# Kernel optimization log

Measured on AMD Instinct MI355X. Metric: run time of the kernel, lower is better.

Reference implementation:

```python
import jax, jax.numpy as jnp
import numpy as np

NUM_HEADS = 32
HEAD_DIM = 32  # hard-coded in the module


def _rope_sincos(seq_len, head_dim):
    # NOTE: module uses arange(0, head_dim)/head_dim (full dim, not the usual /2 stride)
    inv_freq = 1.0 / (10000.0 ** (jnp.arange(0, head_dim, dtype=jnp.float32) / head_dim))
    freqs = jnp.outer(jnp.arange(seq_len, dtype=jnp.float32), inv_freq)  # [S, D]
    # original repeats over heads then reshapes -> identical values per head,
    # so broadcasting with shape [1, S, 1, D] is equivalent.
    return jnp.sin(freqs)[None, :, None, :], jnp.cos(freqs)[None, :, None, :]


def _apply_rope(x, sin, cos):
    x1, x2 = jnp.split(x, 2, axis=-1)
    x_rot = jnp.concatenate([-x2, x1], axis=-1)
    return x * cos + x_rot * sin


def setup_inputs() -> dict:
    key = jax.random.key(0)
    B, S, H, D = 2, 2048, NUM_HEADS, HEAD_DIM
    dm = H * D
    k1, k2 = jax.random.split(key)
    x = jax.random.normal(k1, (B, S, dm), dtype=jnp.float32)
    W_qkv = jax.random.normal(k2, (dm, 3 * dm), dtype=jnp.float32) / np.sqrt(dm).astype(np.float32)
    mask = jnp.tril(jnp.ones((S, S), dtype=bool))[None, None]  # causal, [1,1,S,S]
    return {"x": x, "W_qkv": W_qkv, "mask": mask}


def reference(x, W_qkv, mask):
    B, S, dm = x.shape
    H, D = NUM_HEADS, HEAD_DIM
    qkv = x @ W_qkv  # [B, S, 3*H*D], no bias
    q, k, v = jnp.split(qkv, 3, axis=-1)
    q = q.reshape(B, S, H, D)
    k = k.reshape(B, S, H, D)
    v = v.reshape(B, S, H, D)

    sin, cos = _rope_sincos(S, D)
    q = _apply_rope(q, sin, cos)
    k = _apply_rope(k, sin, cos)

    # [B, H, S, D]
    q = q.transpose(0, 2, 1, 3)
    k = k.transpose(0, 2, 1, 3)
    v = v.transpose(0, 2, 1, 3)

    scale = 1.0 / np.sqrt(D).astype(np.float32)
    attn = jnp.einsum('bhqd,bhkd->bhqk', q, k) * scale  # [B, H, S, S]
    attn = jnp.where(mask, attn, jnp.float32(-jnp.inf))
    attn = jax.nn.softmax(attn, axis=-1)
    out = jnp.einsum('bhqk,bhkd->bhqd', attn, v)  # [B, H, S, D]
    return out.transpose(0, 2, 1, 3).reshape(B, S, H * D)
```

## Files before the change

### kernel.cpp

```cpp
#include <hip/hip_runtime.h>
#include <cstdint>
#include <cstddef>

#define BB 2
#define SS 2048
#define HH 32
#define DD 32
#define DM 1024
#define MROWS 4096
#define NQKV 3072

#define QSCALE 0.25503486f

typedef __attribute__((ext_vector_type(8))) short bf16x8;
typedef __attribute__((ext_vector_type(4))) float f32x4;
typedef __attribute__((address_space(1))) unsigned int gu32;
typedef __attribute__((address_space(3))) unsigned int lu32;

__device__ __forceinline__ unsigned short f2bf(float f) {
    union { float f; unsigned int u; } v;
    v.f = f;
    unsigned int u = v.u;
    u += 0x7fffu + ((u >> 16) & 1u);
    return (unsigned short)(u >> 16);
}

__device__ __forceinline__ unsigned int cvt_pk_bf16(float a, float b) {
    unsigned int r;
    asm("v_cvt_pk_bf16_f32 %0, %1, %2" : "=v"(r) : "v"(a), "v"(b));
    return r;
}
__device__ __forceinline__ unsigned short bf1(float a) {
    return (unsigned short)cvt_pk_bf16(a, a);
}

__global__ __launch_bounds__(256) void prep_k(
        const float* __restrict__ x, const float* __restrict__ w,
        unsigned short* __restrict__ xb, unsigned short* __restrict__ wT,
        float* __restrict__ tk, float* __restrict__ tq) {
    __shared__ unsigned short tile[64][65];
    const int blk = blockIdx.x;
    const int tid = threadIdx.x;
    if (blk < 4096) {
        const int i = blk * 256 + tid;
        float4 v = ((const float4*)x)[i];
        ushort4 o;
        o.x = f2bf(v.x); o.y = f2bf(v.y); o.z = f2bf(v.z); o.w = f2bf(v.w);
        ((ushort4*)xb)[i] = o;
    } else if (blk < 4864) {
        const int bx = blk - 4096;
        const int n0 = (bx % 48) * 64;
        const int k0 = (bx / 48) * 64;
        const int tx = tid & 63;
        const int ty = tid >> 6;
        for (int i = ty; i < 64; i += 4)
            tile[i][tx] = f2bf(w[(size_t)(k0 + i) * NQKV + n0 + tx]);
        __syncthreads();
        for (int i = ty; i < 64; i += 4)
            wT[(size_t)(n0 + i) * 1024 + k0 + tx] = tile[tx][i];
    } else {
        const int i = (blk - 4864) * 256 + tid;
        const int s = i >> 4, dl = i & 15;
        const float inv1 = exp2f((float)dl * -0.41524101186092029f);
        const float inv2 = exp2f((float)(dl + 16) * -0.41524101186092029f);
        float s1, c1, s2, c2;
        sincosf((float)s * inv1, &s1, &c1);
        sincosf((float)s * inv2, &s2, &c2);
        float4 vk = {s1, c1, s2, c2};
        float4 vq = {s1 * QSCALE, c1 * QSCALE, s2 * QSCALE, c2 * QSCALE};
        ((float4*)tk)[i] = vk;
        ((float4*)tq)[i] = vq;
    }
}

__global__ __launch_bounds__(256) void qkv_gemm_k(
        const unsigned short* __restrict__ xb,
        const unsigned short* __restrict__ wTp,
        const float4* __restrict__ tk, const float4* __restrict__ tq,
        unsigned short* __restrict__ qbuf,
        unsigned short* __restrict__ kbuf,
        unsigned short* __restrict__ vtbuf) {
    __shared__ unsigned short smem[2 * 128 * 32];
    unsigned short* As = smem;
    unsigned short* Bs = smem + 4096;
    const int m0 = blockIdx.x * 128;
    const int n0 = blockIdx.y * 128;
    const int tid = threadIdx.x;
    const int w = tid >> 6, lane = tid & 63;
    const int quad = lane >> 4, l16 = lane & 15;
    const int wr = w >> 1, wc = w & 1;

    f32x4 acc[4][4];
#pragma unroll
    for (int i = 0; i < 4; ++i)
#pragma unroll
        for (int j = 0; j < 4; ++j)
            acc[i][j] = (f32x4){0.f, 0.f, 0.f, 0.f};

    const int goff = (lane >> 2) * 1024 + (((lane ^ (lane >> 3)) & 3)) * 8;
    const int Gr = l16 * 4 + quad;
    const int L = Gr ^ ((Gr >> 3) & 3);
    const int roff = L * 8;

    for (int k0 = 0; k0 < 1024; k0 += 32) {
        __syncthreads();
#pragma unroll
        for (int q = 0; q < 2; ++q) {
            const int seg = w * 2 + q;
            const unsigned short* ga = xb  + (size_t)(m0 + seg * 16) * 1024 + k0 + goff;
            const unsigned short* gb = wTp + (size_t)(n0 + seg * 16) * 1024 + k0 + goff;
            __builtin_amdgcn_global_load_lds((gu32*)ga, (lu32*)(As + seg * 512), 16, 0, 0);
            __builtin_amdgcn_global_load_lds((gu32*)gb, (lu32*)(Bs + seg * 512), 16, 0, 0);
        }
        __syncthreads();
        bf16x8 af[4], bfv[4];
#pragma unroll
        for (int i = 0; i < 4; ++i)
            af[i] = *(const bf16x8*)(As + (wr * 4 + i) * 512 + roff);
#pragma unroll
        for (int j = 0; j < 4; ++j)
            bfv[j] = *(const bf16x8*)(Bs + (wc * 4 + j) * 512 + roff);
#pragma unroll
        for (int i = 0; i < 4; ++i)
#pragma unroll
            for (int j = 0; j < 4; ++j)
                acc[i][j] = __builtin_amdgcn_mfma_f32_16x16x32_bf16(af[i], bfv[j], acc[i][j], 0, 0, 0);
    }

    const int sec = n0 >> 10;
    const int rowb = m0 + wr * 64;
    const int colb = n0 + wc * 64;
    if (sec < 2) {
        unsigned short* dst = (sec == 0) ? qbuf : kbuf;
        const float4* tab = (sec == 0) ? tq : tk;
        const int h0 = (colb & 1023) >> 5;
        const int h1 = ((colb + 32) & 1023) >> 5;
#pragma unroll
        for (int i = 0; i < 4; ++i) {
#pragma unroll
            for (int r = 0; r < 4; ++r) {
                const int row = rowb + i * 16 + quad * 4 + r;
                const int bb = row >> 11, s = row & 2047;
                const float4 t = tab[s * 16 + l16];
                unsigned short* pb = dst + ((size_t)(bb * 32) * 2048 + s) * 32;
                {
                    const float x1 = acc[i][0][r], x2 = acc[i][1][r];
                    unsigned short* p = pb + (size_t)h0 * (2048 * 32);
                    p[l16]      = bf1(x1 * t.y - x2 * t.x);
                    p[l16 + 16] = bf1(x2 * t.w + x1 * t.z);
                }
                {
                    const float x1 = acc[i][2][r], x2 = acc[i][3][r];
                    unsigned short* p = pb + (size_t)h1 * (2048 * 32);
                    p[l16]      = bf1(x1 * t.y - x2 * t.x);
                    p[l16 + 16] = bf1(x2 * t.w + x1 * t.z);
                }
            }
        }
    } else {
        __syncthreads();
        unsigned short* tw = smem + w * 2048;
        const int bbi = rowb >> 11;
        const int srow = rowb & 2047;
        const int colB = colb - 2048;
#pragma unroll
        for (int j = 0; j < 4; ++j) {
#pragma unroll
            for (int i = 0; i < 4; ++i) {
                uint2 pk;
                pk.x = cvt_pk_bf16(acc[i][j][0], acc[i][j][1]);
                pk.y = cvt_pk_bf16(acc[i][j][2], acc[i][j][3]);
                *(uint2*)&tw[l16 * 66 + i * 16 + quad * 4] = pk;
            }
#pragma unroll
            for (int c = 0; c < 16; ++c) {
                const int col = colB + j * 16 + c;
                const int hh = col >> 5, d = col & 31;
                vtbuf[((size_t)(bbi * 32 + hh) * 32 + d) * 2048 + srow + lane] = tw[c * 66 + lane];
            }
        }
    }
}

__global__ __launch_bounds__(256) void attn_k(
        const unsigned short* __restrict__ qb,
        const unsigned short* __restrict__ kb,
        const unsigned short* __restrict__ vt,
        float* __restrict__ out) {
    __shared__ unsigned short Pl[4][2][32][40];
    const int tid = threadIdx.x;
    const int w = tid >> 6, lane = tid & 63;
    const int quad = lane >> 4, l16 = lane & 15;
    const int bh = blockIdx.x >> 4;
    const int j = blockIdx.x & 15;
    const int b = bh >> 5, h = bh & 31;

    const int c = (w < 2) ? (2 * j + w) : (62 - 2 * j + (w - 2));
    const int qw = c * 32;
    const int nkt = c + 1;

    const unsigned short* qbase = qb + (size_t)bh * 2048 * 32;
    const unsigned short* kbase = kb + (size_t)bh * 2048 * 32;
    const unsigned short* vbase = vt + (size_t)bh * 32 * 2048;
    const f32x4 fz = {0.f, 0.f, 0.f, 0.f};

    bf16x8 qf0 = *(const bf16x8*)(qbase + (size_t)(qw + l16) * 32 + quad * 8);
    bf16x8 qf1 = *(const bf16x8*)(qbase + (size_t)(qw + 16 + l16) * 32 + quad * 8);

    f32x4 a00 = fz, a01 = fz, a10 = fz, a11 = fz;
    float ls0 = 0.f, ls1 = 0.f;

    const unsigned short* kp0 = kbase + (size_t)l16 * 32 + quad * 8;
    const unsigned short* kp1 = kbase + (size_t)(16 + l16) * 32 + quad * 8;
    const unsigned short* vp0 = vbase + (size_t)l16 * 2048 + quad * 8;
    const unsigned short* vp1 = vbase + (size_t)(16 + l16) * 2048 + quad * 8;

    bf16x8 kc0 = *(const bf16x8*)kp0;
    bf16x8 kc1 = *(const bf16x8*)kp1;
    bf16x8 vc0 = *(const bf16x8*)vp0;
    bf16x8 vc1 = *(const bf16x8*)vp1;

    for (int kt = 0; kt < nkt - 1; ++kt) {
        kp0 += 1024; kp1 += 1024; vp0 += 32; vp1 += 32;
        bf16x8 kn0 = *(const bf16x8*)kp0;
        bf16x8 kn1 = *(const bf16x8*)kp1;
        bf16x8 vn0 = *(const bf16x8*)vp0;
        bf16x8 vn1 = *(const bf16x8*)vp1;

        f32x4 s00 = __builtin_amdgcn_mfma_f32_16x16x32_bf16(kc0, qf0, fz, 0, 0, 0);
        f32x4 s01 = __builtin_amdgcn_mfma_f32_16x16x32_bf16(kc0, qf1, fz, 0, 0, 0);
        f32x4 s10 = __builtin_amdgcn_mfma_f32_16x16x32_bf16(kc1, qf0, fz, 0, 0, 0);
        f32x4 s11 = __builtin_amdgcn_mfma_f32_16x16x32_bf16(kc1, qf1, fz, 0, 0, 0);

        unsigned short (*plw)[40] = Pl[w][kt & 1];
        {
            float p0 = __builtin_amdgcn_exp2f(s00[0]), p1 = __builtin_amdgcn_exp2f(s00[1]);
            float p2 = __builtin_amdgcn_exp2f(s00[2]), p3 = __builtin_amdgcn_exp2f(s00[3]);
            ls0 += (p0 + p1) + (p2 + p3);
            uint2 pk; pk.x = cvt_pk_bf16(p0, p1); pk.y = cvt_pk_bf16(p2, p3);
            *(uint2*)&plw[l16][quad * 4] = pk;
        }
        {
            float p0 = __builtin_amdgcn_exp2f(s01[0]), p1 = __builtin_amdgcn_exp2f(s01[1]);
            float p2 = __builtin_amdgcn_exp2f(s01[2]), p3 = __builtin_amdgcn_exp2f(s01[3]);
            ls1 += (p0 + p1) + (p2 + p3);
            uint2 pk; pk.x = cvt_pk_bf16(p0, p1); pk.y = cvt_pk_bf16(p2, p3);
            *(uint2*)&plw[16 + l16][quad * 4] = pk;
        }
        {
            float p0 = __builtin_amdgcn_exp2f(s10[0]), p1 = __builtin_amdgcn_exp2f(s10[1]);
            float p2 = __builtin_amdgcn_exp2f(s10[2]), p3 = __builtin_amdgcn_exp2f(s10[3]);
            ls0 += (p0 + p1) + (p2 + p3);
            uint2 pk; pk.x = cvt_pk_bf16(p0, p1); pk.y = cvt_pk_bf16(p2, p3);
            *(uint2*)&plw[l16][16 + quad * 4] = pk;
        }
        {
            float p0 = __builtin_amdgcn_exp2f(s11[0]), p1 = __builtin_amdgcn_exp2f(s11[1]);
            float p2 = __builtin_amdgcn_exp2f(s11[2]), p3 = __builtin_amdgcn_exp2f(s11[3]);
            ls1 += (p0 + p1) + (p2 + p3);
            uint2 pk; pk.x = cvt_pk_bf16(p0, p1); pk.y = cvt_pk_bf16(p2, p3);
            *(uint2*)&plw[16 + l16][16 + quad * 4] = pk;
        }

        bf16x8 pf0 = *(const bf16x8*)&plw[l16][quad * 8];
        bf16x8 pf1 = *(const bf16x8*)&plw[16 + l16][quad * 8];
        a00 = __builtin_amdgcn_mfma_f32_16x16x32_bf16(vc0, pf0, a00, 0, 0, 0);
        a01 = __builtin_amdgcn_mfma_f32_16x16x32_bf16(vc0, pf1, a01, 0, 0, 0);
        a10 = __builtin_amdgcn_mfma_f32_16x16x32_bf16(vc1, pf0, a10, 0, 0, 0);
        a11 = __builtin_amdgcn_mfma_f32_16x16x32_bf16(vc1, pf1, a11, 0, 0, 0);

        kc0 = kn0; kc1 = kn1; vc0 = vn0; vc1 = vn1;
    }

    {
        f32x4 s00 = __builtin_amdgcn_mfma_f32_16x16x32_bf16(kc0, qf0, fz, 0, 0, 0);
        f32x4 s01 = __builtin_amdgcn_mfma_f32_16x16x32_bf16(kc0, qf1, fz, 0, 0, 0);
        f32x4 s11 = __builtin_amdgcn_mfma_f32_16x16x32_bf16(kc1, qf1, fz, 0, 0, 0);

        unsigned short (*plw)[40] = Pl[w][(nkt - 1) & 1];
        {
            float p[4];
#pragma unroll
            for (int r = 0; r < 4; ++r)
                p[r] = (quad * 4 + r > l16) ? 0.f : __builtin_amdgcn_exp2f(s00[r]);
            ls0 += (p[0] + p[1]) + (p[2] + p[3]);
            uint2 pk; pk.x = cvt_pk_bf16(p[0], p[1]); pk.y = cvt_pk_bf16(p[2], p[3]);
            *(uint2*)&plw[l16][quad * 4] = pk;
        }
        {
            float p0 = __builtin_amdgcn_exp2f(s01[0]), p1 = __builtin_amdgcn_exp2f(s01[1]);
            float p2 = __builtin_amdgcn_exp2f(s01[2]), p3 = __builtin_amdgcn_exp2f(s01[3]);
            ls1 += (p0 + p1) + (p2 + p3);
            uint2 pk; pk.x = cvt_pk_bf16(p0, p1); pk.y = cvt_pk_bf16(p2, p3);
            *(uint2*)&plw[16 + l16][quad * 4] = pk;
        }
        {
            uint2 pk; pk.x = 0; pk.y = 0;
            *(uint2*)&plw[l16][16 + quad * 4] = pk;
        }
        {
            float p[4];
#pragma unroll
            for (int r = 0; r < 4; ++r)
                p[r] = (quad * 4 + r > l16) ? 0.f : __builtin_amdgcn_exp2f(s11[r]);
            ls1 += (p[0] + p[1]) + (p[2] + p[3]);
            uint2 pk; pk.x = cvt_pk_bf16(p[0], p[1]); pk.y = cvt_pk_bf16(p[2], p[3]);
            *(uint2*)&plw[16 + l16][16 + quad * 4] = pk;
        }

        bf16x8 pf0 = *(const bf16x8*)&plw[l16][quad * 8];
        bf16x8 pf1 = *(const bf16x8*)&plw[16 + l16][quad * 8];
        a00 = __builtin_amdgcn_mfma_f32_16x16x32_bf16(vc0, pf0, a00, 0, 0, 0);
        a01 = __builtin_amdgcn_mfma_f32_16x16x32_bf16(vc0, pf1, a01, 0, 0, 0);
        a10 = __builtin_amdgcn_mfma_f32_16x16x32_bf16(vc1, pf0, a10, 0, 0, 0);
        a11 = __builtin_amdgcn_mfma_f32_16x16x32_bf16(vc1, pf1, a11, 0, 0, 0);
    }

    float l0 = ls0; l0 += __shfl_xor(l0, 16); l0 += __shfl_xor(l0, 32);
    float l1 = ls1; l1 += __shfl_xor(l1, 16); l1 += __shfl_xor(l1, 32);
    const float inv0 = 1.f / l0, inv1 = 1.f / l1;

    float* ot = (float*)&Pl[w][0][0][0];
    {
        f32x4 t;
        t = a00; t[0]*=inv0; t[1]*=inv0; t[2]*=inv0; t[3]*=inv0;
        *(f32x4*)&ot[(l16) * 36 + quad * 4] = t;
        t = a10; t[0]*=inv0; t[1]*=inv0; t[2]*=inv0; t[3]*=inv0;
        *(f32x4*)&ot[(l16) * 36 + 16 + quad * 4] = t;
        t = a01; t[0]*=inv1; t[1]*=inv1; t[2]*=inv1; t[3]*=inv1;
        *(f32x4*)&ot[(16 + l16) * 36 + quad * 4] = t;
        t = a11; t[0]*=inv1; t[1]*=inv1; t[2]*=inv1; t[3]*=inv1;
        *(f32x4*)&ot[(16 + l16) * 36 + 16 + quad * 4] = t;
    }
    const int dd = lane & 31, qpar = lane >> 5;
    float* ob = out + (size_t)(b * 2048 + qw) * 1024 + h * 32;
#pragma unroll
    for (int i2 = 0; i2 < 16; ++i2) {
        const int qloc = i2 * 2 + qpar;
        ob[(size_t)qloc * 1024 + dd] = ot[qloc * 36 + dd];
    }
}

extern "C" void kernel_launch(void* const* d_in, const int* in_sizes, int n_in,
                              void* d_out, int out_size, void* d_ws, size_t ws_size,
                              hipStream_t stream) {
    (void)in_sizes; (void)n_in; (void)out_size; (void)ws_size;
    const float* x = (const float*)d_in[0];
    const float* wq = (const float*)d_in[1];
    float* out = (float*)d_out;

    unsigned short* xb = (unsigned short*)d_ws;
    unsigned short* wT = xb + (size_t)MROWS * DM;
    unsigned short* qb = wT + (size_t)NQKV * DM;
    unsigned short* kb = qb + (size_t)BB * HH * SS * DD;
    unsigned short* vt = kb + (size_t)BB * HH * SS * DD;
    float* tk = (float*)(vt + (size_t)BB * HH * SS * DD);
    float* tq = tk + (size_t)SS * 16 * 4;

    prep_k<<<dim3(4992), dim3(256), 0, stream>>>(x, wq, xb, wT, tk, tq);
    qkv_gemm_k<<<dim3(MROWS / 128, NQKV / 128), dim3(256), 0, stream>>>(
        xb, wT, (const float4*)tk, (const float4*)tq, qb, kb, vt);
    attn_k<<<dim3(BB * HH * 16), dim3(256), 0, stream>>>(qb, kb, vt, out);
}
```

Before: 183.8 us.

## Restructure attention to 16-row query tiles with register P shuffles and MFMA row sums

The attention kernel moves from 32-row query tiles per wave to 16-row tiles, with each wave handling two paired tiles (c and 127-c) for causal load balance. The P matrix is now redistributed between lanes with ds_bpermute instead of an LDS store and reload. Row sums come from an extra MFMA against a ones vector rather than scalar adds and shuffles. The blocks are reordered so the 64 batch-heads are the fast-varying index. The RoPE epilogue of the QKV GEMM also writes packed 32-bit pairs instead of two separate 16-bit stores. Smaller tiles raise parallelism and cut LDS traffic, but K/V reuse per loaded fragment drops and each wave now spends an extra MFMA per step on the sums.

```diff
diff --git a/kernel.cpp b/kernel.cpp
--- a/kernel.cpp
+++ b/kernel.cpp
@@ -29,9 +29,6 @@
     unsigned int r;
     asm("v_cvt_pk_bf16_f32 %0, %1, %2" : "=v"(r) : "v"(a), "v"(b));
     return r;
-}
-__device__ __forceinline__ unsigned short bf1(float a) {
-    return (unsigned short)cvt_pk_bf16(a, a);
 }
 
 __global__ __launch_bounds__(256) void prep_k(
@@ -145,15 +142,13 @@
                 unsigned short* pb = dst + ((size_t)(bb * 32) * 2048 + s) * 32;
                 {
                     const float x1 = acc[i][0][r], x2 = acc[i][1][r];
-                    unsigned short* p = pb + (size_t)h0 * (2048 * 32);
-                    p[l16]      = bf1(x1 * t.y - x2 * t.x);
-                    p[l16 + 16] = bf1(x2 * t.w + x1 * t.z);
+                    unsigned int* p32 = (unsigned int*)(pb + (size_t)h0 * (2048 * 32));
+                    p32[l16] = cvt_pk_bf16(x1 * t.y - x2 * t.x, x2 * t.w + x1 * t.z);
                 }
                 {
                     const float x1 = acc[i][2][r], x2 = acc[i][3][r];
-                    unsigned short* p = pb + (size_t)h1 * (2048 * 32);
-                    p[l16]      = bf1(x1 * t.y - x2 * t.x);
-                    p[l16 + 16] = bf1(x2 * t.w + x1 * t.z);
+                    unsigned int* p32 = (unsigned int*)(pb + (size_t)h1 * (2048 * 32));
+                    p32[l16] = cvt_pk_bf16(x1 * t.y - x2 * t.x, x2 * t.w + x1 * t.z);
                 }
             }
         }
@@ -187,157 +182,152 @@
         const unsigned short* __restrict__ kb,
         const unsigned short* __restrict__ vt,
         float* __restrict__ out) {
-    __shared__ unsigned short Pl[4][2][32][40];
+    __shared__ float ots[4][16 * 36];
     const int tid = threadIdx.x;
     const int w = tid >> 6, lane = tid & 63;
     const int quad = lane >> 4, l16 = lane & 15;
-    const int bh = blockIdx.x >> 4;
-    const int j = blockIdx.x & 15;
+    const int bh = blockIdx.x & 63;
+    const int pg = blockIdx.x >> 6;
+    const int pid = pg * 4 + w;
     const int b = bh >> 5, h = bh & 31;
-
-    const int c = (w < 2) ? (2 * j + w) : (62 - 2 * j + (w - 2));
-    const int qw = c * 32;
-    const int nkt = c + 1;
 
     const unsigned short* qbase = qb + (size_t)bh * 2048 * 32;
     const unsigned short* kbase = kb + (size_t)bh * 2048 * 32;
     const unsigned short* vbase = vt + (size_t)bh * 32 * 2048;
     const f32x4 fz = {0.f, 0.f, 0.f, 0.f};
-
-    bf16x8 qf0 = *(const bf16x8*)(qbase + (size_t)(qw + l16) * 32 + quad * 8);
-    bf16x8 qf1 = *(const bf16x8*)(qbase + (size_t)(qw + 16 + l16) * 32 + quad * 8);
-
-    f32x4 a00 = fz, a01 = fz, a10 = fz, a11 = fz;
-    float ls0 = 0.f, ls1 = 0.f;
-
-    const unsigned short* kp0 = kbase + (size_t)l16 * 32 + quad * 8;
-    const unsigned short* kp1 = kbase + (size_t)(16 + l16) * 32 + quad * 8;
-    const unsigned short* vp0 = vbase + (size_t)l16 * 2048 + quad * 8;
-    const unsigned short* vp1 = vbase + (size_t)(16 + l16) * 2048 + quad * 8;
-
-    bf16x8 kc0 = *(const bf16x8*)kp0;
-    bf16x8 kc1 = *(const bf16x8*)kp1;
-    bf16x8 vc0 = *(const bf16x8*)vp0;
-    bf16x8 vc1 = *(const bf16x8*)vp1;
-
-    for (int kt = 0; kt < nkt - 1; ++kt) {
-        kp0 += 1024; kp1 += 1024; vp0 += 32; vp1 += 32;
-        bf16x8 kn0 = *(const bf16x8*)kp0;
-        bf16x8 kn1 = *(const bf16x8*)kp1;
-        bf16x8 vn0 = *(const bf16x8*)vp0;
-        bf16x8 vn1 = *(const bf16x8*)vp1;
-
-        f32x4 s00 = __builtin_amdgcn_mfma_f32_16x16x32_bf16(kc0, qf0, fz, 0, 0, 0);
-        f32x4 s01 = __builtin_amdgcn_mfma_f32_16x16x32_bf16(kc0, qf1, fz, 0, 0, 0);
-        f32x4 s10 = __builtin_amdgcn_mfma_f32_16x16x32_bf16(kc1, qf0, fz, 0, 0, 0);
-        f32x4 s11 = __builtin_amdgcn_mfma_f32_16x16x32_bf16(kc1, qf1, fz, 0, 0, 0);
-
-        unsigned short (*plw)[40] = Pl[w][kt & 1];
+    const short one = (short)0x3F80;
+    const bf16x8 ones8 = {one, one, one, one, one, one, one, one};
+
+    const int koffA = l16 * 32 + quad * 8;
+    const int koffB = (16 + l16) * 32 + quad * 8;
+    const int voff0 = l16 * 2048 + quad * 8;
+    const int voff1 = (16 + l16) * 2048 + quad * 8;
+    const int addrA = (((quad & 1) << 5) + l16) << 2;
+    const int addrB = addrA + 64;
+    const bool hi = quad >= 2;
+    const int dd = lane & 31, qpar = lane >> 5;
+
+#pragma unroll
+    for (int ph = 0; ph < 2; ++ph) {
+        const int c = ph ? (127 - pid) : pid;
+        bf16x8 qf = *(const bf16x8*)(qbase + (size_t)((c << 4) + l16) * 32 + quad * 8);
+
+        f32x4 a0 = fz, a1 = fz, lacc = fz;
+
+        const unsigned short* kp = kbase;
+        const unsigned short* vp = vbase;
+        bf16x8 kcA = *(const bf16x8*)(kp + koffA);
+        bf16x8 kcB = *(const bf16x8*)(kp + koffB);
+        bf16x8 v0c = *(const bf16x8*)(vp + voff0);
+        bf16x8 v1c = *(const bf16x8*)(vp + voff1);
+
+        const int np = c >> 1;
+        for (int t = 0; t < np; ++t) {
+            kp += 1024; vp += 32;
+            bf16x8 knA = *(const bf16x8*)(kp + koffA);
+            bf16x8 knB = *(const bf16x8*)(kp + koffB);
+            bf16x8 v0n = *(const bf16x8*)(vp + voff0);
+            bf16x8 v1n = *(const bf16x8*)(vp + voff1);
+
+            f32x4 sA = __builtin_amdgcn_mfma_f32_16x16x32_bf16(kcA, qf, fz, 0, 0, 0);
+            f32x4 sB = __builtin_amdgcn_mfma_f32_16x16x32_bf16(kcB, qf, fz, 0, 0, 0);
+            unsigned int uA0 = cvt_pk_bf16(__builtin_amdgcn_exp2f(sA[0]), __builtin_amdgcn_exp2f(sA[1]));
+            unsigned int uA1 = cvt_pk_bf16(__builtin_amdgcn_exp2f(sA[2]), __builtin_amdgcn_exp2f(sA[3]));
+            unsigned int uB0 = cvt_pk_bf16(__builtin_amdgcn_exp2f(sB[0]), __builtin_amdgcn_exp2f(sB[1]));
+            unsigned int uB1 = cvt_pk_bf16(__builtin_amdgcn_exp2f(sB[2]), __builtin_amdgcn_exp2f(sB[3]));
+
+            int w0a = __builtin_amdgcn_ds_bpermute(addrA, (int)uA0);
+            int w0b = __builtin_amdgcn_ds_bpermute(addrA, (int)uB0);
+            int w1a = __builtin_amdgcn_ds_bpermute(addrA, (int)uA1);
+            int w1b = __builtin_amdgcn_ds_bpermute(addrA, (int)uB1);
+            int w2a = __builtin_amdgcn_ds_bpermute(addrB, (int)uA0);
+            int w2b = __builtin_amdgcn_ds_bpermute(addrB, (int)uB0);
+            int w3a = __builtin_amdgcn_ds_bpermute(addrB, (int)uA1);
+            int w3b = __builtin_amdgcn_ds_bpermute(addrB, (int)uB1);
+            uint4 wv;
+            wv.x = (unsigned int)(hi ? w0b : w0a);
+            wv.y = (unsigned int)(hi ? w1b : w1a);
+            wv.z = (unsigned int)(hi ? w2b : w2a);
+            wv.w = (unsigned int)(hi ? w3b : w3a);
+            bf16x8 pf = __builtin_bit_cast(bf16x8, wv);
+
+            a0   = __builtin_amdgcn_mfma_f32_16x16x32_bf16(v0c, pf, a0, 0, 0, 0);
+            a1   = __builtin_amdgcn_mfma_f32_16x16x32_bf16(v1c, pf, a1, 0, 0, 0);
+            lacc = __builtin_amdgcn_mfma_f32_16x16x32_bf16(ones8, pf, lacc, 0, 0, 0);
+
+            kcA = knA; kcB = knB; v0c = v0n; v1c = v1n;
+        }
+
+        if (c & 1) {
+            f32x4 sA = __builtin_amdgcn_mfma_f32_16x16x32_bf16(kcA, qf, fz, 0, 0, 0);
+            f32x4 sB = __builtin_amdgcn_mfma_f32_16x16x32_bf16(kcB, qf, fz, 0, 0, 0);
+            float pB[4];
+#pragma unroll
+            for (int r = 0; r < 4; ++r)
+                pB[r] = (quad * 4 + r > l16) ? 0.f : __builtin_amdgcn_exp2f(sB[r]);
+            unsigned int uA0 = cvt_pk_bf16(__builtin_amdgcn_exp2f(sA[0]), __builtin_amdgcn_exp2f(sA[1]));
+            unsigned int uA1 = cvt_pk_bf16(__builtin_amdgcn_exp2f(sA[2]), __builtin_amdgcn_exp2f(sA[3]));
+            unsigned int uB0 = cvt_pk_bf16(pB[0], pB[1]);
+            unsigned int uB1 = cvt_pk_bf16(pB[2], pB[3]);
+
+            int w0a = __builtin_amdgcn_ds_bpermute(addrA, (int)uA0);
+            int w0b = __builtin_amdgcn_ds_bpermute(addrA, (int)uB0);
+            int w1a = __builtin_amdgcn_ds_bpermute(addrA, (int)uA1);
+            int w1b = __builtin_amdgcn_ds_bpermute(addrA, (int)uB1);
+            int w2a = __builtin_amdgcn_ds_bpermute(addrB, (int)uA0);
+            int w2b = __builtin_amdgcn_ds_bpermute(addrB, (int)uB0);
+            int w3a = __builtin_amdgcn_ds_bpermute(addrB, (int)uA1);
+            int w3b = __builtin_amdgcn_ds_bpermute(addrB, (int)uB1);
+            uint4 wv;
+            wv.x = (unsigned int)(hi ? w0b : w0a);
+            wv.y = (unsigned int)(hi ? w1b : w1a);
+            wv.z = (unsigned int)(hi ? w2b : w2a);
+            wv.w = (unsigned int)(hi ? w3b : w3a);
+            bf16x8 pf = __builtin_bit_cast(bf16x8, wv);
+
+            a0   = __builtin_amdgcn_mfma_f32_16x16x32_bf16(v0c, pf, a0, 0, 0, 0);
+            a1   = __builtin_amdgcn_mfma_f32_16x16x32_bf16(v1c, pf, a1, 0, 0, 0);
+            lacc = __builtin_amdgcn_mfma_f32_16x16x32_bf16(ones8, pf, lacc, 0, 0, 0);
+        } else {
+            f32x4 sA = __builtin_amdgcn_mfma_f32_16x16x32_bf16(kcA, qf, fz, 0, 0, 0);
+            float pA[4];
+#pragma unroll
+            for (int r = 0; r < 4; ++r)
+                pA[r] = (quad * 4 + r > l16) ? 0.f : __builtin_amdgcn_exp2f(sA[r]);
+            unsigned int uA0 = cvt_pk_bf16(pA[0], pA[1]);
+            unsigned int uA1 = cvt_pk_bf16(pA[2], pA[3]);
+
+            int w0a = __builtin_amdgcn_ds_bpermute(addrA, (int)uA0);
+            int w1a = __builtin_amdgcn_ds_bpermute(addrA, (int)uA1);
+            int w2a = __builtin_amdgcn_ds_bpermute(addrB, (int)uA0);
+            int w3a = __builtin_amdgcn_ds_bpermute(addrB, (int)uA1);
+            uint4 wv;
+            wv.x = hi ? 0u : (unsigned int)w0a;
+            wv.y = hi ? 0u : (unsigned int)w1a;
+            wv.z = hi ? 0u : (unsigned int)w2a;
+            wv.w = hi ? 0u : (unsigned int)w3a;
+            bf16x8 pf = __builtin_bit_cast(bf16x8, wv);
+
+            a0   = __builtin_amdgcn_mfma_f32_16x16x32_bf16(v0c, pf, a0, 0, 0, 0);
+            a1   = __builtin_amdgcn_mfma_f32_16x16x32_bf16(v1c, pf, a1, 0, 0, 0);
+            lacc = __builtin_amdgcn_mfma_f32_16x16x32_bf16(ones8, pf, lacc, 0, 0, 0);
+        }
+
+        const float inv = 1.f / lacc[0];
+        float* ot = ots[w];
         {
-            float p0 = __builtin_amdgcn_exp2f(s00[0]), p1 = __builtin_amdgcn_exp2f(s00[1]);
-            float p2 = __builtin_amdgcn_exp2f(s00[2]), p3 = __builtin_amdgcn_exp2f(s00[3]);
-            ls0 += (p0 + p1) + (p2 + p3);
-            uint2 pk; pk.x = cvt_pk_bf16(p0, p1); pk.y = cvt_pk_bf16(p2, p3);
-            *(uint2*)&plw[l16][quad * 4] = pk;
-        }
-        {
-            float p0 = __builtin_amdgcn_exp2f(s01[0]), p1 = __builtin_amdgcn_exp2f(s01[1]);
-            float p2 = __builtin_amdgcn_exp2f(s01[2]), p3 = __builtin_amdgcn_exp2f(s01[3]);
-            ls1 += (p0 + p1) + (p2 + p3);
-            uint2 pk; pk.x = cvt_pk_bf16(p0, p1); pk.y = cvt_pk_bf16(p2, p3);
-            *(uint2*)&plw[16 + l16][quad * 4] = pk;
-        }
-        {
-            float p0 = __builtin_amdgcn_exp2f(s10[0]), p1 = __builtin_amdgcn_exp2f(s10[1]);
-            float p2 = __builtin_amdgcn_exp2f(s10[2]), p3 = __builtin_amdgcn_exp2f(s10[3]);
-            ls0 += (p0 + p1) + (p2 + p3);
-            uint2 pk; pk.x = cvt_pk_bf16(p0, p1); pk.y = cvt_pk_bf16(p2, p3);
-            *(uint2*)&plw[l16][16 + quad * 4] = pk;
-        }
-        {
-            float p0 = __builtin_amdgcn_exp2f(s11[0]), p1 = __builtin_amdgcn_exp2f(s11[1]);
-            float p2 = __builtin_amdgcn_exp2f(s11[2]), p3 = __builtin_amdgcn_exp2f(s11[3]);
-            ls1 += (p0 + p1) + (p2 + p3);
-            uint2 pk; pk.x = cvt_pk_bf16(p0, p1); pk.y = cvt_pk_bf16(p2, p3);
-            *(uint2*)&plw[16 + l16][16 + quad * 4] = pk;
-        }
-
-        bf16x8 pf0 = *(const bf16x8*)&plw[l16][quad * 8];
-        bf16x8 pf1 = *(const bf16x8*)&plw[16 + l16][quad * 8];
-        a00 = __builtin_amdgcn_mfma_f32_16x16x32_bf16(vc0, pf0, a00, 0, 0, 0);
-        a01 = __builtin_amdgcn_mfma_f32_16x16x32_bf16(vc0, pf1, a01, 0, 0, 0);
-        a10 = __builtin_amdgcn_mfma_f32_16x16x32_bf16(vc1, pf0, a10, 0, 0, 0);
-        a11 = __builtin_amdgcn_mfma_f32_16x16x32_bf16(vc1, pf1, a11, 0, 0, 0);
-
-        kc0 = kn0; kc1 = kn1; vc0 = vn0; vc1 = vn1;
-    }
-
-    {
-        f32x4 s00 = __builtin_amdgcn_mfma_f32_16x16x32_bf16(kc0, qf0, fz, 0, 0, 0);
-        f32x4 s01 = __builtin_amdgcn_mfma_f32_16x16x32_bf16(kc0, qf1, fz, 0, 0, 0);
-        f32x4 s11 = __builtin_amdgcn_mfma_f32_16x16x32_bf16(kc1, qf1, fz, 0, 0, 0);
-
-        unsigned short (*plw)[40] = Pl[w][(nkt - 1) & 1];
-        {
-            float p[4];
-#pragma unroll
-            for (int r = 0; r < 4; ++r)
-                p[r] = (quad * 4 + r > l16) ? 0.f : __builtin_amdgcn_exp2f(s00[r]);
-            ls0 += (p[0] + p[1]) + (p[2] + p[3]);
-            uint2 pk; pk.x = cvt_pk_bf16(p[0], p[1]); pk.y = cvt_pk_bf16(p[2], p[3]);
-            *(uint2*)&plw[l16][quad * 4] = pk;
-        }
-        {
-            float p0 = __builtin_amdgcn_exp2f(s01[0]), p1 = __builtin_amdgcn_exp2f(s01[1]);
-            float p2 = __builtin_amdgcn_exp2f(s01[2]), p3 = __builtin_amdgcn_exp2f(s01[3]);
-            ls1 += (p0 + p1) + (p2 + p3);
-            uint2 pk; pk.x = cvt_pk_bf16(p0, p1); pk.y = cvt_pk_bf16(p2, p3);
-            *(uint2*)&plw[16 + l16][quad * 4] = pk;
-        }
-        {
-            uint2 pk; pk.x = 0; pk.y = 0;
-            *(uint2*)&plw[l16][16 + quad * 4] = pk;
-        }
-        {
-            float p[4];
-#pragma unroll
-            for (int r = 0; r < 4; ++r)
-                p[r] = (quad * 4 + r > l16) ? 0.f : __builtin_amdgcn_exp2f(s11[r]);
-            ls1 += (p[0] + p[1]) + (p[2] + p[3]);
-            uint2 pk; pk.x = cvt_pk_bf16(p[0], p[1]); pk.y = cvt_pk_bf16(p[2], p[3]);
-            *(uint2*)&plw[16 + l16][16 + quad * 4] = pk;
-        }
-
-        bf16x8 pf0 = *(const bf16x8*)&plw[l16][quad * 8];
-        bf16x8 pf1 = *(const bf16x8*)&plw[16 + l16][quad * 8];
-        a00 = __builtin_amdgcn_mfma_f32_16x16x32_bf16(vc0, pf0, a00, 0, 0, 0);
-        a01 = __builtin_amdgcn_mfma_f32_16x16x32_bf16(vc0, pf1, a01, 0, 0, 0);
-        a10 = __builtin_amdgcn_mfma_f32_16x16x32_bf16(vc1, pf0, a10, 0, 0, 0);
-        a11 = __builtin_amdgcn_mfma_f32_16x16x32_bf16(vc1, pf1, a11, 0, 0, 0);
-    }
-
-    float l0 = ls0; l0 += __shfl_xor(l0, 16); l0 += __shfl_xor(l0, 32);
-    float l1 = ls1; l1 += __shfl_xor(l1, 16); l1 += __shfl_xor(l1, 32);
-    const float inv0 = 1.f / l0, inv1 = 1.f / l1;
-
-    float* ot = (float*)&Pl[w][0][0][0];
-    {
-        f32x4 t;
-        t = a00; t[0]*=inv0; t[1]*=inv0; t[2]*=inv0; t[3]*=inv0;
-        *(f32x4*)&ot[(l16) * 36 + quad * 4] = t;
-        t = a10; t[0]*=inv0; t[1]*=inv0; t[2]*=inv0; t[3]*=inv0;
-        *(f32x4*)&ot[(l16) * 36 + 16 + quad * 4] = t;
-        t = a01; t[0]*=inv1; t[1]*=inv1; t[2]*=inv1; t[3]*=inv1;
-        *(f32x4*)&ot[(16 + l16) * 36 + quad * 4] = t;
-        t = a11; t[0]*=inv1; t[1]*=inv1; t[2]*=inv1; t[3]*=inv1;
-        *(f32x4*)&ot[(16 + l16) * 36 + 16 + quad * 4] = t;
-    }
-    const int dd = lane & 31, qpar = lane >> 5;
-    float* ob = out + (size_t)(b * 2048 + qw) * 1024 + h * 32;
-#pragma unroll
-    for (int i2 = 0; i2 < 16; ++i2) {
-        const int qloc = i2 * 2 + qpar;
-        ob[(size_t)qloc * 1024 + dd] = ot[qloc * 36 + dd];
+            f32x4 t;
+            t[0] = a0[0] * inv; t[1] = a0[1] * inv; t[2] = a0[2] * inv; t[3] = a0[3] * inv;
+            *(f32x4*)&ot[l16 * 36 + quad * 4] = t;
+            t[0] = a1[0] * inv; t[1] = a1[1] * inv; t[2] = a1[2] * inv; t[3] = a1[3] * inv;
+            *(f32x4*)&ot[l16 * 36 + 16 + quad * 4] = t;
+        }
+        float* ob = out + (size_t)(b * 2048 + (c << 4)) * 1024 + h * 32;
+#pragma unroll
+        for (int i2 = 0; i2 < 8; ++i2) {
+            const int qloc = i2 * 2 + qpar;
+            ob[(size_t)qloc * 1024 + dd] = ot[qloc * 36 + dd];
+        }
     }
 }
 
@@ -360,5 +350,5 @@
     prep_k<<<dim3(4992), dim3(256), 0, stream>>>(x, wq, xb, wT, tk, tq);
     qkv_gemm_k<<<dim3(MROWS / 128, NQKV / 128), dim3(256), 0, stream>>>(
         xb, wT, (const float4*)tk, (const float4*)tq, qb, kb, vt);
-    attn_k<<<dim3(BB * HH * 16), dim3(256), 0, stream>>>(qb, kb, vt, out);
-}
+    attn_k<<<dim3(1024), dim3(256), 0, stream>>>(qb, kb, vt, out);
+}
```

New measurement: 223.4 us. +21.5%, slower.
